# Kernel tuning notes

Measured on AMD Instinct MI355X. Metric: run time of the kernel, lower is better.

Reference implementation:

```python
import jax, jax.numpy as jnp
import numpy as np
from jax import lax

N = 100000   # total nodes in batched graph
E = 3200000  # total edges
B = 32       # graphs in batch
L = 1000     # text sequence length (required by mx3 kernel=108)
D = 128      # emb_dim
H = 3        # heads of gcn1
OD = 128     # output_dim


def setup_inputs() -> dict:
    key = jax.random.key(0)
    ks = jax.random.split(key, 32)
    def p(i, shape, s=0.05):
        return jax.random.normal(ks[i], shape, jnp.float32) * s
    return {
        "node_feat": p(0, (N, D), 1.0),
        "src": jax.random.randint(ks[1], (E,), 0, N),
        "dst": jax.random.randint(ks[2], (E,), 0, N),
        "graph_ids": jnp.sort(jax.random.randint(ks[3], (N,), 0, B)),
        "pad_dmap": p(4, (B, 1, L, D), 1.0),
        # GATConv 1: in=D, out=D, heads=3
        "W1": p(5, (D, H * D)), "al1": p(6, (H, D)), "ar1": p(7, (H, D)), "b1": p(8, (H * D,)),
        # GATConv 2: in=3D, out=3D, heads=1
        "W2": p(9, (H * D, H * D)), "al2": p(10, (1, H * D)), "ar2": p(11, (1, H * D)), "b2": p(12, (H * D,)),
        "fc_g1_w": p(13, (H * D, OD)), "fc_g1_b": p(14, (OD,)),
        # Conv1d weights in torch OIH layout
        "conv1_w": p(15, (128, D, 3)), "conv1_b": p(16, (128,)),
        "conv2_w": p(17, (128, 128, 3)), "conv2_b": p(18, (128,)),
        "conv3_w": p(19, (128, 128, 3)), "conv3_b": p(20, (128,)),
        "tf_w": p(21, (128, OD)), "tf_b": p(22, (OD,)),
        "w1": jnp.array([0.5], jnp.float32),
        "fc1_w": p(23, (OD, 512)), "fc1_b": p(24, (512,)),
        "fc2_w": p(25, (512, 256)), "fc2_b": p(26, (256,)),
        "out_w": p(27, (256, 2)), "out_b": p(28, (2,)),
    }


def _gat(feat, src, dst, W, al, ar, b, heads, od):
    """DGL GATConv (feat_drop=attn_drop=0, negative_slope=0.2, bias)."""
    n = feat.shape[0]
    h = (feat @ W).reshape(n, heads, od)                 # [N,H,od]
    el = jnp.einsum('nhd,hd->nh', h, al)                 # [N,H]
    er = jnp.einsum('nhd,hd->nh', h, ar)
    e = jax.nn.leaky_relu(el[src] + er[dst], 0.2)        # [E,H] per-edge score
    m = jax.ops.segment_max(e, dst, num_segments=n)
    m = jnp.where(jnp.isfinite(m), m, 0.0)               # isolated nodes -> 0
    a = jnp.exp(e - m[dst])
    s = jax.ops.segment_sum(a, dst, num_segments=n)
    alpha = a / s[dst]                                   # edge softmax over in-neighborhood
    rst = jax.ops.segment_sum(alpha[:, :, None] * h[src], dst, num_segments=n)
    return rst + b.reshape(1, heads, od)


def _conv1d(x, w, b):
    y = lax.conv_general_dilated(x, w, (1,), 'VALID', dimension_numbers=('NCH', 'OIH', 'NCH'))
    return y + b[None, :, None]


def _maxpool1d(x, k, s):
    return lax.reduce_window(x, -jnp.inf, lax.max, (1, 1, k), (1, 1, s), 'VALID')


def reference(node_feat, src, dst, graph_ids, pad_dmap,
              W1, al1, ar1, b1, W2, al2, ar2, b2,
              fc_g1_w, fc_g1_b, conv1_w, conv1_b, conv2_w, conv2_b,
              conv3_w, conv3_b, tf_w, tf_b, w1,
              fc1_w, fc1_b, fc2_w, fc2_b, out_w, out_b):
    relu = jax.nn.relu
    # graph branch
    g = relu(_gat(node_feat, src, dst, W1, al1, ar1, b1, H, D)).reshape(-1, H * D)
    g = relu(_gat(g, src, dst, W2, al2, ar2, b2, 1, H * D)).reshape(-1, H * D)
    gpool = jax.ops.segment_max(g, graph_ids, num_segments=B)   # graph max pooling [B,384]
    g1 = relu(gpool @ fc_g1_w + fc_g1_b)
    # text CNN branch
    x = pad_dmap[:, 0].transpose(0, 2, 1)                       # [B, D, L]
    f = _maxpool1d(_conv1d(x, conv1_w, conv1_b), 3, 3)
    f = _maxpool1d(_conv1d(f, conv2_w, conv2_b), 3, 3)
    f = _maxpool1d(_conv1d(f, conv3_w, conv3_b), 108, 1)[:, :, 0]  # [B,128]
    seq1 = relu(f @ tf_w + tf_b)
    # weighted fusion + MLP head (dropout is identity in eval)
    wv = jax.nn.sigmoid(w1)
    gc = (1.0 - wv) * g1 + wv * seq1
    gc = relu(gc @ fc1_w + fc1_b)
    gc = relu(gc @ fc2_w + fc2_b)
    o = relu(gc @ out_w + out_b)
    return jax.nn.softmax(o, axis=1)
```

## Files before the change

kernel.cpp:

```cpp
#include <hip/hip_runtime.h>
#include <math.h>

constexpr int NN = 100000;
constexpr int EE = 3200000;
constexpr int BB = 32;
constexpr int LSEQ = 1000;
constexpr int DD = 128;
constexpr int NH = 3;
constexpr int HD = 384;
constexpr int NB1 = (NN + 255) / 256;
constexpr int NMT = (NN + 127) / 128;

typedef __attribute__((ext_vector_type(8))) short bf16v8;
typedef __attribute__((ext_vector_type(4))) float f32x4;

static __device__ __forceinline__ float lrelu(float x) { return x > 0.f ? x : 0.2f * x; }
static __device__ __forceinline__ float bf2f(unsigned short u) {
  return __uint_as_float(((unsigned)u) << 16);
}
static __device__ __forceinline__ unsigned short f2bf(float f) {
  unsigned x = __float_as_uint(f);
  return (unsigned short)((x + 0x7fffu + ((x >> 16) & 1u)) >> 16);
}

constexpr int PB_NF   = (NN * DD / 4) / 256;
constexpr int PB_PAD  = (BB * LSEQ * 128 / 4) / 256;
constexpr int PB_DEG  = NB1;
constexpr int PB_GP   = (BB * HD + 255) / 256;
constexpr int PB_TW1  = (128 * 384 + 255) / 256;
constexpr int PB_TW2  = (384 * 384 + 255) / 256;
constexpr int PB_TC   = (128 * 384 + 255) / 256;
constexpr int PREP_BLOCKS = PB_NF + PB_PAD + PB_DEG + PB_GP + PB_TW1 + PB_TW2 + 3 * PB_TC;

__global__ void prep_misc(const float* __restrict__ nf, unsigned short* __restrict__ nfbf,
                          const float* __restrict__ pad, unsigned short* __restrict__ padbf,
                          int* __restrict__ deg, unsigned* __restrict__ gpool,
                          const float* __restrict__ W1, unsigned short* __restrict__ Wt1,
                          const float* __restrict__ W2, unsigned short* __restrict__ Wt2,
                          const float* __restrict__ c1w, unsigned short* __restrict__ Wc1,
                          const float* __restrict__ c2w, unsigned short* __restrict__ Wc2,
                          const float* __restrict__ c3w, unsigned short* __restrict__ Wc3) {
  int bx = blockIdx.x, tid = threadIdx.x;
  if (bx < PB_NF) {
    int i = bx * 256 + tid;
    float4 v = ((const float4*)nf)[i];
    ushort4 o;
    o.x = f2bf(v.x); o.y = f2bf(v.y); o.z = f2bf(v.z); o.w = f2bf(v.w);
    ((ushort4*)nfbf)[i] = o;
    return;
  }
  bx -= PB_NF;
  if (bx < PB_PAD) {
    int i = bx * 256 + tid;
    float4 v = ((const float4*)pad)[i];
    ushort4 o;
    o.x = f2bf(v.x); o.y = f2bf(v.y); o.z = f2bf(v.z); o.w = f2bf(v.w);
    ((ushort4*)padbf)[i] = o;
    return;
  }
  bx -= PB_PAD;
  if (bx < PB_DEG) {
    int i = bx * 256 + tid;
    if (i < NN) deg[i] = 0;
    return;
  }
  bx -= PB_DEG;
  if (bx < PB_GP) {
    int i = bx * 256 + tid;
    if (i < BB * HD) gpool[i] = 0u;
    return;
  }
  bx -= PB_GP;
  if (bx < PB_TW1) {
    int id = bx * 256 + tid;
    if (id < 384 * 128) { int n = id / 128, k = id % 128; Wt1[id] = f2bf(W1[(size_t)k * 384 + n]); }
    return;
  }
  bx -= PB_TW1;
  if (bx < PB_TW2) {
    int id = bx * 256 + tid;
    if (id < 384 * 384) { int n = id / 384, k = id % 384; Wt2[id] = f2bf(W2[(size_t)k * 384 + n]); }
    return;
  }
  bx -= PB_TW2;
  const float* cw = (bx < PB_TC) ? c1w : (bx < 2 * PB_TC) ? c2w : c3w;
  unsigned short* co = (bx < PB_TC) ? Wc1 : (bx < 2 * PB_TC) ? Wc2 : Wc3;
  int id = (bx % PB_TC) * 256 + tid;
  if (id < 128 * 384) {
    int o = id / 384, rem = id % 384;
    int t = rem / 128, i = rem % 128;
    co[id] = f2bf(cw[(size_t)o * 384 + i * 3 + t]);
  }
}

__global__ void hist_k(const int* __restrict__ dst, int* __restrict__ deg) {
  int i = blockIdx.x * 256 + threadIdx.x;
  if (i >= EE / 4) return;
  int4 d = ((const int4*)dst)[i];
  atomicAdd(&deg[d.x], 1);
  atomicAdd(&deg[d.y], 1);
  atomicAdd(&deg[d.z], 1);
  atomicAdd(&deg[d.w], 1);
}

__global__ void scan1_k(const int* __restrict__ deg, int* __restrict__ excl,
                        int* __restrict__ bsum) {
  __shared__ int tmp[256];
  int tid = threadIdx.x;
  int i = blockIdx.x * 256 + tid;
  int v = (i < NN) ? deg[i] : 0;
  tmp[tid] = v;
  __syncthreads();
  for (int off = 1; off < 256; off <<= 1) {
    int t = (tid >= off) ? tmp[tid - off] : 0;
    __syncthreads();
    tmp[tid] += t;
    __syncthreads();
  }
  if (i < NN) excl[i] = tmp[tid] - v;
  if (tid == 255) bsum[blockIdx.x] = tmp[255];
}

__global__ void scan2p(int* __restrict__ bsum) {
  __shared__ int tmp[512];
  int tid = threadIdx.x;
  int v = (tid < NB1) ? bsum[tid] : 0;
  tmp[tid] = v;
  __syncthreads();
  for (int off = 1; off < 512; off <<= 1) {
    int t = (tid >= off) ? tmp[tid - off] : 0;
    __syncthreads();
    tmp[tid] += t;
    __syncthreads();
  }
  if (tid < NB1) bsum[tid] = tmp[tid] - v;
}

__global__ void scan3_k(const int* __restrict__ excl, const int* __restrict__ bsum,
                        int* __restrict__ offs, int* __restrict__ cursor) {
  int i = blockIdx.x * 256 + threadIdx.x;
  if (i < NN) {
    int o = excl[i] + bsum[blockIdx.x];
    offs[i] = o;
    cursor[i] = o;
  }
}

__global__ void scatter_k(const int* __restrict__ src, const int* __restrict__ dst,
                          int* __restrict__ cursor, int* __restrict__ srcs) {
  int i = blockIdx.x * 256 + threadIdx.x;
  if (i >= EE / 4) return;
  int4 s = ((const int4*)src)[i];
  int4 d = ((const int4*)dst)[i];
  srcs[atomicAdd(&cursor[d.x], 1)] = s.x;
  srcs[atomicAdd(&cursor[d.y], 1)] = s.y;
  srcs[atomicAdd(&cursor[d.z], 1)] = s.z;
  srcs[atomicAdd(&cursor[d.w], 1)] = s.w;
}

template <int NKB, bool BRES>
__global__ __launch_bounds__(512) void gemm_nres(const unsigned short* __restrict__ A,
                                                 const unsigned short* __restrict__ Bt,
                                                 unsigned short* __restrict__ C,
                                                 int M, int Nc, int nmt, int mpb) {
  static_assert(!BRES || NKB <= 2, "resident B needs K<=128");
  constexpr int KTOT = NKB * 64;
  __shared__ unsigned short As[2][8192];
  __shared__ unsigned short Bs[16384];
  int tid = threadIdx.x;
  int lane = tid & 63;
  int wave = tid >> 6;
  int wm = wave >> 2, wn = wave & 3;
  int tile_n = blockIdx.x * 128;
  int rloc = lane >> 3;
  int cs = (lane & 7) ^ rloc;
  const unsigned short* Bb = Bt + (size_t)tile_n * KTOT;

  int mt0 = blockIdx.y * mpb;
  if (mt0 >= nmt) return;
  int mt1 = min(mt0 + mpb, nmt);

  auto stage_a = [&](int mt, int kb, int buf) {
    const unsigned short* Ab = A + (size_t)mt * 128 * KTOT;
    int mr = M - 1 - mt * 128;
#pragma unroll
    for (int q = 0; q < 2; ++q) {
      int t = wave * 2 + q, r = t * 8 + rloc;
      int ra = r > mr ? mr : r;
      __builtin_amdgcn_global_load_lds(
          (const __attribute__((address_space(1))) void*)(Ab + (size_t)ra * KTOT + kb * 64 + cs * 8),
          (__attribute__((address_space(3))) void*)(&As[buf][t * 512]), 16, 0, 0);
    }
  };
  auto stage_b = [&](int kb, int buf) {
#pragma unroll
    for (int q = 0; q < 2; ++q) {
      int t = wave * 2 + q, r = t * 8 + rloc;
      __builtin_amdgcn_global_load_lds(
          (const __attribute__((address_space(1))) void*)(Bb + (size_t)r * KTOT + kb * 64 + cs * 8),
          (__attribute__((address_space(3))) void*)(&Bs[buf * 8192 + t * 512]), 16, 0, 0);
    }
  };

  f32x4 acc[4][2];
#pragma unroll
  for (int i = 0; i < 4; ++i)
#pragma unroll
    for (int j = 0; j < 2; ++j) acc[i][j] = (f32x4){0.f, 0.f, 0.f, 0.f};

  if constexpr (BRES) {
#pragma unroll
    for (int kb = 0; kb < NKB; ++kb) stage_b(kb, kb);
  } else {
    stage_b(0, 0);
  }
  stage_a(mt0, 0, 0);
  __syncthreads();

  int nsteps = (mt1 - mt0) * NKB;
  for (int i = 0; i < nsteps; ++i) {
    int mt = mt0 + i / NKB;
    int kb = i % NKB;
    int cb = i & 1;
    if (i + 1 < nsteps) {
      int ni = i + 1;
      stage_a(mt0 + ni / NKB, ni % NKB, ni & 1);
      if constexpr (!BRES) stage_b(ni % NKB, ni & 1);
    }
    const unsigned short* Ablk = &As[cb][0];
    const unsigned short* Bblk = BRES ? (Bs + kb * 8192) : (Bs + cb * 8192);
#pragma unroll
    for (int ks = 0; ks < 2; ++ks) {
      int q = ks * 4 + (lane >> 4);
      bf16v8 af[4], bfr[2];
#pragma unroll
      for (int ii = 0; ii < 4; ++ii) {
        int r = wm * 64 + ii * 16 + (lane & 15);
        af[ii] = *(const bf16v8*)&Ablk[r * 64 + ((q ^ (r & 7)) * 8)];
      }
#pragma unroll
      for (int j = 0; j < 2; ++j) {
        int r = wn * 32 + j * 16 + (lane & 15);
        bfr[j] = *(const bf16v8*)&Bblk[r * 64 + ((q ^ (r & 7)) * 8)];
      }
#pragma unroll
      for (int ii = 0; ii < 4; ++ii)
#pragma unroll
        for (int j = 0; j < 2; ++j)
          acc[ii][j] = __builtin_amdgcn_mfma_f32_16x16x32_bf16(af[ii], bfr[j], acc[ii][j], 0, 0, 0);
    }
    if (kb == NKB - 1) {
#pragma unroll
      for (int ii = 0; ii < 4; ++ii) {
        int row0 = mt * 128 + wm * 64 + ii * 16 + (lane >> 4) * 4;
#pragma unroll
        for (int j = 0; j < 2; ++j) {
          int col = tile_n + wn * 32 + j * 16 + (lane & 15);
#pragma unroll
          for (int p = 0; p < 4; ++p) {
            int row = row0 + p;
            if (row < M) C[(size_t)row * Nc + col] = f2bf(acc[ii][j][p]);
          }
          acc[ii][j] = (f32x4){0.f, 0.f, 0.f, 0.f};
        }
      }
    }
    __syncthreads();
  }
}

__global__ __launch_bounds__(256) void gemm_mfma(const unsigned short* __restrict__ A,
                                                 int lda,
                                                 const unsigned short* __restrict__ Bt,
                                                 unsigned short* __restrict__ C,
                                                 int M, int K, int Nc,
                                                 const float* __restrict__ bias,
                                                 long aBatch, long cBatch) {
  __shared__ unsigned short As[128 * 64];
  __shared__ unsigned short Bs[128 * 64];
  int lane = threadIdx.x & 63;
  int wave = threadIdx.x >> 6;
  int wm = wave >> 1, wn = wave & 1;
  int tile_m = blockIdx.y * 128;
  int tile_n = blockIdx.x * 128;
  int maxRa = M - 1 - tile_m;
  f32x4 acc[4][4];
#pragma unroll
  for (int i = 0; i < 4; ++i)
#pragma unroll
    for (int j = 0; j < 4; ++j) acc[i][j] = (f32x4){0.f, 0.f, 0.f, 0.f};

  const unsigned short* Ab = A + (size_t)blockIdx.z * aBatch + (size_t)tile_m * lda;
  unsigned short* Cb = C + (size_t)blockIdx.z * cBatch;
  const unsigned short* Bb = Bt + (size_t)tile_n * K;
  int rloc = (lane >> 3);
  int cs = (lane & 7) ^ rloc;

  for (int k0 = 0; k0 < K; k0 += 64) {
#pragma unroll
    for (int q = 0; q < 4; ++q) {
      int t = wave * 4 + q;
      int r = t * 8 + rloc;
      int ra = r > maxRa ? maxRa : r;
      __builtin_amdgcn_global_load_lds(
          (const __attribute__((address_space(1))) void*)(Ab + (size_t)ra * lda + k0 + cs * 8),
          (__attribute__((address_space(3))) void*)(As + t * 512), 16, 0, 0);
      __builtin_amdgcn_global_load_lds(
          (const __attribute__((address_space(1))) void*)(Bb + (size_t)r * K + k0 + cs * 8),
          (__attribute__((address_space(3))) void*)(Bs + t * 512), 16, 0, 0);
    }
    __syncthreads();
#pragma unroll
    for (int ks = 0; ks < 2; ++ks) {
      int q = ks * 4 + (lane >> 4);
      bf16v8 af[4], bfr[4];
#pragma unroll
      for (int i = 0; i < 4; ++i) {
        int r = wm * 64 + i * 16 + (lane & 15);
        af[i] = *(const bf16v8*)&As[r * 64 + ((q ^ (r & 7)) * 8)];
      }
#pragma unroll
      for (int j = 0; j < 4; ++j) {
        int r = wn * 64 + j * 16 + (lane & 15);
        bfr[j] = *(const bf16v8*)&Bs[r * 64 + ((q ^ (r & 7)) * 8)];
      }
#pragma unroll
      for (int i = 0; i < 4; ++i)
#pragma unroll
        for (int j = 0; j < 4; ++j)
          acc[i][j] = __builtin_amdgcn_mfma_f32_16x16x32_bf16(af[i], bfr[j], acc[i][j], 0, 0, 0);
    }
    __syncthreads();
  }
#pragma unroll
  for (int i = 0; i < 4; ++i) {
    int row0 = tile_m + wm * 64 + i * 16 + (lane >> 4) * 4;
#pragma unroll
    for (int j = 0; j < 4; ++j) {
      int col = tile_n + wn * 64 + j * 16 + (lane & 15);
      float bv = bias ? bias[col] : 0.f;
#pragma unroll
      for (int p = 0; p < 4; ++p) {
        int row = row0 + p;
        if (row < M) Cb[(size_t)row * Nc + col] = f2bf(acc[i][j][p] + bv);
      }
    }
  }
}

__global__ void elr_k1(const unsigned short* __restrict__ h, const float* __restrict__ al,
                       const float* __restrict__ ar, float* __restrict__ el,
                       float* __restrict__ er) {
  int wid = (blockIdx.x * 256 + threadIdx.x) >> 6;
  int lane = threadIdx.x & 63;
  if (wid >= NN * NH) return;
  int n = wid / NH, hh = wid % NH;
  const unsigned short* row = h + (size_t)n * HD + hh * DD;
  const float* a = al + hh * DD;
  const float* r = ar + hh * DD;
  int c = lane * 2;
  unsigned v = *(const unsigned*)(row + c);
  float x0 = bf2f((unsigned short)(v & 0xffffu));
  float x1 = bf2f((unsigned short)(v >> 16));
  float pel = x0 * a[c] + x1 * a[c + 1];
  float per = x0 * r[c] + x1 * r[c + 1];
#pragma unroll
  for (int off = 32; off; off >>= 1) {
    pel += __shfl_down(pel, off);
    per += __shfl_down(per, off);
  }
  if (lane == 0) { el[n * 4 + hh] = pel; er[n * 4 + hh] = per; }
}

__global__ void elr_k2(const unsigned short* __restrict__ h, const float* __restrict__ al,
                       const float* __restrict__ ar, float* __restrict__ el,
                       float* __restrict__ er) {
  int wid = (blockIdx.x * 256 + threadIdx.x) >> 6;
  int lane = threadIdx.x & 63;
  if (wid >= NN) return;
  const unsigned short* row = h + (size_t)wid * HD;
  float pel = 0.f, per = 0.f;
#pragma unroll
  for (int k = 0; k < 3; ++k) {
    int c = lane * 2 + k * 128;
    unsigned v = *(const unsigned*)(row + c);
    float x0 = bf2f((unsigned short)(v & 0xffffu));
    float x1 = bf2f((unsigned short)(v >> 16));
    pel += x0 * al[c] + x1 * al[c + 1];
    per += x0 * ar[c] + x1 * ar[c + 1];
  }
#pragma unroll
  for (int off = 32; off; off >>= 1) {
    pel += __shfl_down(pel, off);
    per += __shfl_down(per, off);
  }
  if (lane == 0) { el[wid] = pel; er[wid] = per; }
}

template <int H>
static __device__ __forceinline__ void agg_body3(const float4 t,
                                                 const unsigned short* __restrict__ hfeat,
                                                 int lane, float acc[6]) {
  int s2 = __float_as_int(t.w);
  const unsigned short* hrow = hfeat + (size_t)s2 * HD;
  uint2 va = *(const uint2*)(hrow + lane * 4);
  unsigned vb = *(const unsigned*)(hrow + 256 + lane * 2);
  float wa = (H == 3) ? ((lane < 32) ? t.x : t.y) : t.x;
  float wc = (H == 3) ? t.z : t.x;
  acc[0] += wa * bf2f((unsigned short)(va.x & 0xffffu));
  acc[1] += wa * bf2f((unsigned short)(va.x >> 16));
  acc[2] += wa * bf2f((unsigned short)(va.y & 0xffffu));
  acc[3] += wa * bf2f((unsigned short)(va.y >> 16));
  acc[4] += wc * bf2f((unsigned short)(vb & 0xffffu));
  acc[5] += wc * bf2f((unsigned short)(vb >> 16));
}

template <int H>
static __device__ __forceinline__ void load_sc(const float* __restrict__ el,
                                               int s, const float erd[H], float sc[H]) {
  if constexpr (H == 3) {
    float4 e = ((const float4*)el)[s];
    sc[0] = lrelu(e.x + erd[0]);
    sc[1] = lrelu(e.y + erd[1]);
    sc[2] = lrelu(e.z + erd[2]);
  } else {
    sc[0] = lrelu(el[s] + erd[0]);
  }
}

template <int H>
__global__ __launch_bounds__(256) void agg_csr3(const int* __restrict__ offs,
                                                const int* __restrict__ deg,
                                                const int* __restrict__ srcs,
                                                const float* __restrict__ el,
                                                const float* __restrict__ er,
                                                const unsigned short* __restrict__ hfeat,
                                                const float* __restrict__ bias,
                                                unsigned short* __restrict__ outg) {
  __shared__ float wb[4][64][4];
  int wave = threadIdx.x >> 6, lane = threadIdx.x & 63;
  int d = blockIdx.x * 4 + wave;
  int o0 = offs[d], dg = deg[d];
  float erd[H];
  if constexpr (H == 3) {
    float4 e = ((const float4*)er)[d];
    erd[0] = e.x; erd[1] = e.y; erd[2] = e.z;
  } else {
    erd[0] = er[d];
  }
  float acc[6] = {0.f, 0.f, 0.f, 0.f, 0.f, 0.f};
  float wsum[H];
#pragma unroll
  for (int h = 0; h < H; ++h) wsum[h] = 0.f;

  if (dg <= 64) {
    bool has = lane < dg;
    int s = has ? srcs[o0 + lane] : 0;
    float sc[H], mh[H];
    load_sc<H>(el, s, erd, sc);
#pragma unroll
    for (int h = 0; h < H; ++h) {
      if (!has) sc[h] = -1e30f;
      mh[h] = sc[h];
#pragma unroll
      for (int off = 1; off < 64; off <<= 1) mh[h] = fmaxf(mh[h], __shfl_xor(mh[h], off));
    }
    float w0 = 0.f, w1 = 0.f, w2 = 0.f;
    if (has) {
      w0 = __expf(sc[0] - mh[0]);
      if constexpr (H == 3) {
        w1 = __expf(sc[1] - mh[1]);
        w2 = __expf(sc[2] - mh[2]);
      }
    }
    wsum[0] = w0;
    if constexpr (H == 3) { wsum[1] = w1; wsum[2] = w2; }
    *(float4*)&wb[wave][lane][0] = make_float4(w0, w1, w2, __int_as_float(s));
#pragma unroll 16
    for (int j = 0; j < dg; ++j) {
      float4 t = *(const float4*)&wb[wave][j][0];
      agg_body3<H>(t, hfeat, lane, acc);
    }
  } else {
    float mh[H];
#pragma unroll
    for (int h = 0; h < H; ++h) mh[h] = -1e30f;
    for (int e = lane; e < dg; e += 64) {
      int s = srcs[o0 + e];
      float sc[H];
      load_sc<H>(el, s, erd, sc);
#pragma unroll
      for (int h = 0; h < H; ++h) mh[h] = fmaxf(mh[h], sc[h]);
    }
#pragma unroll
    for (int h = 0; h < H; ++h) {
#pragma unroll
      for (int off = 1; off < 64; off <<= 1) mh[h] = fmaxf(mh[h], __shfl_xor(mh[h], off));
    }
    int nch = (dg + 63) >> 6;
    for (int ch = 0; ch < nch; ++ch) {
      int e = ch * 64 + lane;
      bool has = e < dg;
      int s = has ? srcs[o0 + e] : 0;
      float sc[H];
      load_sc<H>(el, s, erd, sc);
      float w0 = 0.f, w1 = 0.f, w2 = 0.f;
      if (has) {
        w0 = __expf(sc[0] - mh[0]);
        if constexpr (H == 3) {
          w1 = __expf(sc[1] - mh[1]);
          w2 = __expf(sc[2] - mh[2]);
        }
      }
      wsum[0] += w0;
      if constexpr (H == 3) { wsum[1] += w1; wsum[2] += w2; }
      *(float4*)&wb[wave][lane][0] = make_float4(w0, w1, w2, __int_as_float(s));
      int cnt = min(64, dg - ch * 64);
#pragma unroll 16
      for (int j = 0; j < cnt; ++j) {
        float4 t = *(const float4*)&wb[wave][j][0];
        agg_body3<H>(t, hfeat, lane, acc);
      }
    }
  }
#pragma unroll
  for (int h = 0; h < H; ++h) {
#pragma unroll
    for (int off = 1; off < 64; off <<= 1) wsum[h] += __shfl_xor(wsum[h], off);
  }
  float swA = (H == 3) ? ((lane < 32) ? wsum[0] : wsum[1]) : wsum[0];
  float swC = (H == 3) ? wsum[H - 1] : wsum[0];
  float invA = (dg > 0) ? 1.f / swA : 0.f;
  float invC = (dg > 0) ? 1.f / swC : 0.f;
  unsigned short* orow = outg + (size_t)d * HD;
  int cA = lane * 4, cB = 256 + lane * 2;
  float r0 = fmaxf(acc[0] * invA + bias[cA + 0], 0.f);
  float r1 = fmaxf(acc[1] * invA + bias[cA + 1], 0.f);
  float r2 = fmaxf(acc[2] * invA + bias[cA + 2], 0.f);
  float r3 = fmaxf(acc[3] * invA + bias[cA + 3], 0.f);
  float r4 = fmaxf(acc[4] * invC + bias[cB + 0], 0.f);
  float r5 = fmaxf(acc[5] * invC + bias[cB + 1], 0.f);
  uint2 pa;
  pa.x = (unsigned)f2bf(r0) | ((unsigned)f2bf(r1) << 16);
  pa.y = (unsigned)f2bf(r2) | ((unsigned)f2bf(r3) << 16);
  *(uint2*)(orow + cA) = pa;
  *(unsigned*)(orow + cB) = (unsigned)f2bf(r4) | ((unsigned)f2bf(r5) << 16);
}

__global__ void graph_pool(const unsigned short* __restrict__ g, const int* __restrict__ gid,
                           unsigned* __restrict__ gp) {
  int c = threadIdx.x;
  int n0 = blockIdx.x * 64;
  int nend = min(n0 + 64, NN);
  int cur = gid[n0];
  float mx = 0.f;
  for (int n = n0; n < nend; ++n) {
    int gg = gid[n];
    if (gg != cur) {
      atomicMax(&gp[cur * HD + c], __float_as_uint(mx));
      cur = gg; mx = 0.f;
    }
    mx = fmaxf(mx, bf2f(g[(size_t)n * HD + c]));
  }
  atomicMax(&gp[cur * HD + c], __float_as_uint(mx));
}

__global__ void maxpool_nhc(const unsigned short* __restrict__ in, unsigned short* __restrict__ out,
                            int Lin, int Lout, int total) {
  int idx = blockIdx.x * 256 + threadIdx.x;
  if (idx >= total) return;
  int c = idx & 127;
  int j = (idx >> 7) % Lout;
  int b = idx / (128 * Lout);
  const unsigned short* p = in + ((size_t)b * Lin + j * 3) * 128 + c;
  float m = bf2f(p[0]);
  m = fmaxf(m, bf2f(p[128]));
  m = fmaxf(m, bf2f(p[256]));
  out[idx] = f2bf(m);
}

__global__ void gpool_c3(const unsigned short* __restrict__ in, float* __restrict__ fvec) {
  int idx = blockIdx.x * 256 + threadIdx.x;
  if (idx >= BB * 128) return;
  int c = idx & 127, b = idx >> 7;
  const unsigned short* p = in + (size_t)b * 108 * 128 + c;
  float m = bf2f(p[0]);
  for (int t = 1; t < 108; ++t) m = fmaxf(m, bf2f(p[t * 128]));
  fvec[idx] = m;
}

__global__ __launch_bounds__(256) void head_all(const unsigned* __restrict__ gpool,
                                                const float* __restrict__ fvec,
                                                const float* __restrict__ fcgw,
                                                const float* __restrict__ fcgb,
                                                const float* __restrict__ tfw,
                                                const float* __restrict__ tfb,
                                                const float* __restrict__ w1s,
                                                const float* __restrict__ fc1w,
                                                const float* __restrict__ fc1b,
                                                const float* __restrict__ fc2w,
                                                const float* __restrict__ fc2b,
                                                const float* __restrict__ outw,
                                                const float* __restrict__ outb,
                                                float* __restrict__ out) {
  __shared__ float gl[HD];
  __shared__ float gcv[128];
  __shared__ float gc1[512];
  __shared__ float gc2[256];
  int b = blockIdx.x, tid = threadIdx.x;
  for (int c = tid; c < HD; c += 256) gl[c] = __uint_as_float(gpool[b * HD + c]);
  __syncthreads();
  float wv = 1.f / (1.f + __expf(-w1s[0]));
  if (tid < 128) {
    float a = fcgb[tid];
    for (int k = 0; k < HD; ++k) a += gl[k] * fcgw[(size_t)k * 128 + tid];
    float g1 = fmaxf(a, 0.f);
    float s = tfb[tid];
    const float* fv = fvec + b * 128;
    for (int k = 0; k < 128; ++k) s += fv[k] * tfw[(size_t)k * 128 + tid];
    float s1 = fmaxf(s, 0.f);
    gcv[tid] = (1.f - wv) * g1 + wv * s1;
  }
  __syncthreads();
#pragma unroll
  for (int q = 0; q < 2; ++q) {
    int j = tid + q * 256;
    float a = fc1b[j];
    for (int k = 0; k < 128; ++k) a += gcv[k] * fc1w[(size_t)k * 512 + j];
    gc1[j] = fmaxf(a, 0.f);
  }
  __syncthreads();
  {
    float a = fc2b[tid];
    for (int k = 0; k < 512; ++k) a += gc1[k] * fc2w[(size_t)k * 256 + tid];
    gc2[tid] = fmaxf(a, 0.f);
  }
  __syncthreads();
  if (tid < 64) {
    float p0 = 0.f, p1 = 0.f;
#pragma unroll
    for (int q = 0; q < 4; ++q) {
      float v = gc2[tid + q * 64];
      p0 += v * outw[(tid + q * 64) * 2 + 0];
      p1 += v * outw[(tid + q * 64) * 2 + 1];
    }
#pragma unroll
    for (int off = 32; off; off >>= 1) {
      p0 += __shfl_down(p0, off);
      p1 += __shfl_down(p1, off);
    }
    if (tid == 0) {
      float o0 = fmaxf(p0 + outb[0], 0.f), o1 = fmaxf(p1 + outb[1], 0.f);
      float mm = fmaxf(o0, o1);
      float e0 = __expf(o0 - mm), e1 = __expf(o1 - mm);
      float inv = 1.f / (e0 + e1);
      out[b * 2 + 0] = e0 * inv;
      out[b * 2 + 1] = e1 * inv;
    }
  }
}

extern "C" void kernel_launch(void* const* d_in, const int* in_sizes, int n_in,
                              void* d_out, int out_size, void* d_ws, size_t ws_size,
                              hipStream_t stream) {
  const float* node_feat = (const float*)d_in[0];
  const int*   src  = (const int*)d_in[1];
  const int*   dst  = (const int*)d_in[2];
  const int*   gids = (const int*)d_in[3];
  const float* pad  = (const float*)d_in[4];
  const float* W1   = (const float*)d_in[5];
  const float* al1  = (const float*)d_in[6];
  const float* ar1  = (const float*)d_in[7];
  const float* b1   = (const float*)d_in[8];
  const float* W2   = (const float*)d_in[9];
  const float* al2  = (const float*)d_in[10];
  const float* ar2  = (const float*)d_in[11];
  const float* b2   = (const float*)d_in[12];
  const float* fcgw = (const float*)d_in[13];
  const float* fcgb = (const float*)d_in[14];
  const float* c1w  = (const float*)d_in[15];
  const float* c1b  = (const float*)d_in[16];
  const float* c2w  = (const float*)d_in[17];
  const float* c2b  = (const float*)d_in[18];
  const float* c3w  = (const float*)d_in[19];
  const float* c3b  = (const float*)d_in[20];
  const float* tfw  = (const float*)d_in[21];
  const float* tfb  = (const float*)d_in[22];
  const float* w1s  = (const float*)d_in[23];
  const float* fc1w = (const float*)d_in[24];
  const float* fc1b = (const float*)d_in[25];
  const float* fc2w = (const float*)d_in[26];
  const float* fc2b = (const float*)d_in[27];
  const float* outw = (const float*)d_in[28];
  const float* outb = (const float*)d_in[29];
  float* out = (float*)d_out;
  char* base = (char*)d_ws;

  constexpr size_t SZ_BIG = (size_t)NN * HD * 2;
  unsigned short* hA = (unsigned short*)(base + 0);
  unsigned short* gB = (unsigned short*)(base + SZ_BIG);
  unsigned short* nfbf = gB;
  size_t o = 2 * SZ_BIG;
  unsigned short* Wt1 = (unsigned short*)(base + o); o += 384 * 128 * 2;
  unsigned short* Wt2 = (unsigned short*)(base + o); o += 384 * 384 * 2;
  unsigned short* Wc1 = (unsigned short*)(base + o); o += 128 * 384 * 2;
  unsigned short* Wc2 = (unsigned short*)(base + o); o += 128 * 384 * 2;
  unsigned short* Wc3 = (unsigned short*)(base + o); o += 128 * 384 * 2;
  int* deg    = (int*)(base + o); o += (size_t)NN * 4;
  int* offs   = (int*)(base + o); o += (size_t)NN * 4;
  int* cursor = (int*)(base + o); o += (size_t)NN * 4;
  int* excl   = (int*)(base + o); o += (size_t)NN * 4;
  int* bsum   = (int*)(base + o); o += 2048;
  int* srcs   = (int*)(base + o); o += (size_t)EE * 4;
  float* el1  = (float*)(base + o); o += (size_t)NN * 4 * 4;
  float* er1  = (float*)(base + o); o += (size_t)NN * 4 * 4;
  float* el2  = (float*)(base + o); o += (size_t)NN * 4;
  float* er2  = (float*)(base + o); o += (size_t)NN * 4;
  unsigned* gpool = (unsigned*)(base + o); o += (size_t)BB * HD * 4;
  float* fvec = (float*)(base + o); o += BB * 128 * 4;

  unsigned short* padbf = (unsigned short*)base;
  unsigned short* c1bf  = padbf + (size_t)BB * LSEQ * 128;
  unsigned short* p1bf  = c1bf + (size_t)BB * 998 * 128;
  unsigned short* c2bf  = p1bf + (size_t)BB * 332 * 128;
  unsigned short* p2bf  = c2bf + (size_t)BB * 330 * 128;
  unsigned short* c3bf  = p2bf + (size_t)BB * 110 * 128;

  prep_misc<<<PREP_BLOCKS, 256, 0, stream>>>(node_feat, nfbf, pad, padbf, deg, gpool,
                                             W1, Wt1, W2, Wt2, c1w, Wc1, c2w, Wc2, c3w, Wc3);

  gemm_mfma<<<dim3(1, 8, BB), 256, 0, stream>>>(padbf, 128, Wc1, c1bf, 998, 384, 128, c1b,
                                                (long)LSEQ * 128, (long)998 * 128);
  maxpool_nhc<<<(BB * 332 * 128 + 255) / 256, 256, 0, stream>>>(c1bf, p1bf, 998, 332, BB * 332 * 128);
  gemm_mfma<<<dim3(1, 3, BB), 256, 0, stream>>>(p1bf, 128, Wc2, c2bf, 330, 384, 128, c2b,
                                                (long)332 * 128, (long)330 * 128);
  maxpool_nhc<<<(BB * 110 * 128 + 255) / 256, 256, 0, stream>>>(c2bf, p2bf, 330, 110, BB * 110 * 128);
  gemm_mfma<<<dim3(1, 1, BB), 256, 0, stream>>>(p2bf, 128, Wc3, c3bf, 108, 384, 128, c3b,
                                                (long)110 * 128, (long)108 * 128);
  gpool_c3<<<(BB * 128 + 255) / 256, 256, 0, stream>>>(c3bf, fvec);

  hist_k<<<EE / 1024, 256, 0, stream>>>(dst, deg);
  scan1_k<<<NB1, 256, 0, stream>>>(deg, excl, bsum);
  scan2p<<<1, 512, 0, stream>>>(bsum);
  scan3_k<<<NB1, 256, 0, stream>>>(excl, bsum, offs, cursor);
  scatter_k<<<EE / 1024, 256, 0, stream>>>(src, dst, cursor, srcs);

  gemm_nres<2, true><<<dim3(3, (NMT + 9) / 10), 512, 0, stream>>>(nfbf, Wt1, hA, NN, HD, NMT, 10);
  elr_k1<<<(NN * NH * 64 + 255) / 256, 256, 0, stream>>>(hA, al1, ar1, el1, er1);
  agg_csr3<3><<<NN / 4, 256, 0, stream>>>(offs, deg, srcs, el1, er1, hA, b1, gB);

  gemm_nres<6, false><<<dim3(3, (NMT + 9) / 10), 512, 0, stream>>>(gB, Wt2, hA, NN, HD, NMT, 10);
  elr_k2<<<(NN * 64 + 255) / 256, 256, 0, stream>>>(hA, al2, ar2, el2, er2);
  agg_csr3<1><<<NN / 4, 256, 0, stream>>>(offs, deg, srcs, el2, er2, hA, b2, gB);

  graph_pool<<<(NN + 63) / 64, 384, 0, stream>>>(gB, gids, gpool);
  head_all<<<BB, 256, 0, stream>>>(gpool, fvec, fcgw, fcgb, tfw, tfb, w1s,
                                   fc1w, fc1b, fc2w, fc2b, outw, outb, out);
}
```

Before: 1.466 ms.

## Fuse attention logit projections into GEMM epilogue and drop scatter atomics via rank

The el/er attention projections are now computed in the GAT GEMM epilogue from the fp32 accumulators, using shuffle reductions and a shared-memory cross-wave sum. This removes the two separate elr kernels that re-read the bf16 hidden features. For the second layer, partial sums from the three column blocks are combined with float atomics into el2/er2, which are now zeroed in the prep kernel. Separately, the histogram kernel records each edge's atomic return value as a rank, so the scatter no longer needs atomics or a cursor array. The cost is an extra 12.8MB rank array written and read, plus an added __syncthreads and epilogue work per tile.

```diff
diff --git a/kernel.cpp b/kernel.cpp
--- a/kernel.cpp
+++ b/kernel.cpp
@@ -26,15 +26,17 @@
 constexpr int PB_NF   = (NN * DD / 4) / 256;
 constexpr int PB_PAD  = (BB * LSEQ * 128 / 4) / 256;
 constexpr int PB_DEG  = NB1;
+constexpr int PB_EL2  = (2 * NN + 255) / 256;
 constexpr int PB_GP   = (BB * HD + 255) / 256;
 constexpr int PB_TW1  = (128 * 384 + 255) / 256;
 constexpr int PB_TW2  = (384 * 384 + 255) / 256;
 constexpr int PB_TC   = (128 * 384 + 255) / 256;
-constexpr int PREP_BLOCKS = PB_NF + PB_PAD + PB_DEG + PB_GP + PB_TW1 + PB_TW2 + 3 * PB_TC;
+constexpr int PREP_BLOCKS = PB_NF + PB_PAD + PB_DEG + PB_EL2 + PB_GP + PB_TW1 + PB_TW2 + 3 * PB_TC;
 
 __global__ void prep_misc(const float* __restrict__ nf, unsigned short* __restrict__ nfbf,
                           const float* __restrict__ pad, unsigned short* __restrict__ padbf,
-                          int* __restrict__ deg, unsigned* __restrict__ gpool,
+                          int* __restrict__ deg, float* __restrict__ el2z,
+                          unsigned* __restrict__ gpool,
                           const float* __restrict__ W1, unsigned short* __restrict__ Wt1,
                           const float* __restrict__ W2, unsigned short* __restrict__ Wt2,
                           const float* __restrict__ c1w, unsigned short* __restrict__ Wc1,
@@ -65,6 +67,12 @@
     return;
   }
   bx -= PB_DEG;
+  if (bx < PB_EL2) {
+    int i = bx * 256 + tid;
+    if (i < 2 * NN) el2z[i] = 0.f;
+    return;
+  }
+  bx -= PB_EL2;
   if (bx < PB_GP) {
     int i = bx * 256 + tid;
     if (i < BB * HD) gpool[i] = 0u;
@@ -93,14 +101,17 @@
   }
 }
 
-__global__ void hist_k(const int* __restrict__ dst, int* __restrict__ deg) {
+__global__ void hist_k(const int* __restrict__ dst, int* __restrict__ deg,
+                       int* __restrict__ rank) {
   int i = blockIdx.x * 256 + threadIdx.x;
   if (i >= EE / 4) return;
   int4 d = ((const int4*)dst)[i];
-  atomicAdd(&deg[d.x], 1);
-  atomicAdd(&deg[d.y], 1);
-  atomicAdd(&deg[d.z], 1);
-  atomicAdd(&deg[d.w], 1);
+  int4 r;
+  r.x = atomicAdd(&deg[d.x], 1);
+  r.y = atomicAdd(&deg[d.y], 1);
+  r.z = atomicAdd(&deg[d.z], 1);
+  r.w = atomicAdd(&deg[d.w], 1);
+  ((int4*)rank)[i] = r;
 }
 
 __global__ void scan1_k(const int* __restrict__ deg, int* __restrict__ excl,
@@ -137,36 +148,40 @@
 }
 
 __global__ void scan3_k(const int* __restrict__ excl, const int* __restrict__ bsum,
-                        int* __restrict__ offs, int* __restrict__ cursor) {
+                        int* __restrict__ offs) {
   int i = blockIdx.x * 256 + threadIdx.x;
-  if (i < NN) {
-    int o = excl[i] + bsum[blockIdx.x];
-    offs[i] = o;
-    cursor[i] = o;
-  }
+  if (i < NN) offs[i] = excl[i] + bsum[blockIdx.x];
 }
 
 __global__ void scatter_k(const int* __restrict__ src, const int* __restrict__ dst,
-                          int* __restrict__ cursor, int* __restrict__ srcs) {
+                          const int* __restrict__ rank, const int* __restrict__ offs,
+                          int* __restrict__ srcs) {
   int i = blockIdx.x * 256 + threadIdx.x;
   if (i >= EE / 4) return;
   int4 s = ((const int4*)src)[i];
   int4 d = ((const int4*)dst)[i];
-  srcs[atomicAdd(&cursor[d.x], 1)] = s.x;
-  srcs[atomicAdd(&cursor[d.y], 1)] = s.y;
-  srcs[atomicAdd(&cursor[d.z], 1)] = s.z;
-  srcs[atomicAdd(&cursor[d.w], 1)] = s.w;
+  int4 r = ((const int4*)rank)[i];
+  srcs[offs[d.x] + r.x] = s.x;
+  srcs[offs[d.y] + r.y] = s.y;
+  srcs[offs[d.z] + r.z] = s.z;
+  srcs[offs[d.w] + r.w] = s.w;
 }
 
 template <int NKB, bool BRES>
 __global__ __launch_bounds__(512) void gemm_nres(const unsigned short* __restrict__ A,
                                                  const unsigned short* __restrict__ Bt,
                                                  unsigned short* __restrict__ C,
+                                                 const float* __restrict__ al,
+                                                 const float* __restrict__ ar,
+                                                 float* __restrict__ el,
+                                                 float* __restrict__ er,
                                                  int M, int Nc, int nmt, int mpb) {
   static_assert(!BRES || NKB <= 2, "resident B needs K<=128");
   constexpr int KTOT = NKB * 64;
   __shared__ unsigned short As[2][8192];
   __shared__ unsigned short Bs[16384];
+  __shared__ float elbuf[128][4];
+  __shared__ float erbuf[128][4];
   int tid = threadIdx.x;
   int lane = tid & 63;
   int wave = tid >> 6;
@@ -175,6 +190,10 @@
   int rloc = lane >> 3;
   int cs = (lane & 7) ^ rloc;
   const unsigned short* Bb = Bt + (size_t)tile_n * KTOT;
+
+  int c0 = tile_n + wn * 32 + (lane & 15);
+  float alv0 = al[c0], alv1 = al[c0 + 16];
+  float arv0 = ar[c0], arv1 = ar[c0 + 16];
 
   int mt0 = blockIdx.y * mpb;
   if (mt0 >= nmt) return;
@@ -261,9 +280,45 @@
             int row = row0 + p;
             if (row < M) C[(size_t)row * Nc + col] = f2bf(acc[ii][j][p]);
           }
-          acc[ii][j] = (f32x4){0.f, 0.f, 0.f, 0.f};
         }
       }
+#pragma unroll
+      for (int ii = 0; ii < 4; ++ii) {
+#pragma unroll
+        for (int p = 0; p < 4; ++p) {
+          float pe = acc[ii][0][p] * alv0 + acc[ii][1][p] * alv1;
+          float pr = acc[ii][0][p] * arv0 + acc[ii][1][p] * arv1;
+#pragma unroll
+          for (int off = 1; off < 16; off <<= 1) {
+            pe += __shfl_xor(pe, off);
+            pr += __shfl_xor(pr, off);
+          }
+          if ((lane & 15) == 0) {
+            int rl = wm * 64 + ii * 16 + (lane >> 4) * 4 + p;
+            elbuf[rl][wn] = pe;
+            erbuf[rl][wn] = pr;
+          }
+        }
+      }
+      __syncthreads();
+      if (tid < 128) {
+        int row = mt * 128 + tid;
+        if (row < M) {
+          float ev = elbuf[tid][0] + elbuf[tid][1] + elbuf[tid][2] + elbuf[tid][3];
+          float rv = erbuf[tid][0] + erbuf[tid][1] + erbuf[tid][2] + erbuf[tid][3];
+          if constexpr (BRES) {
+            el[row * 4 + blockIdx.x] = ev;
+            er[row * 4 + blockIdx.x] = rv;
+          } else {
+            atomicAdd(&el[row], ev);
+            atomicAdd(&er[row], rv);
+          }
+        }
+      }
+#pragma unroll
+      for (int ii = 0; ii < 4; ++ii)
+#pragma unroll
+        for (int j = 0; j < 2; ++j) acc[ii][j] = (f32x4){0.f, 0.f, 0.f, 0.f};
     }
     __syncthreads();
   }
@@ -346,55 +401,6 @@
       }
     }
   }
-}
-
-__global__ void elr_k1(const unsigned short* __restrict__ h, const float* __restrict__ al,
-                       const float* __restrict__ ar, float* __restrict__ el,
-                       float* __restrict__ er) {
-  int wid = (blockIdx.x * 256 + threadIdx.x) >> 6;
-  int lane = threadIdx.x & 63;
-  if (wid >= NN * NH) return;
-  int n = wid / NH, hh = wid % NH;
-  const unsigned short* row = h + (size_t)n * HD + hh * DD;
-  const float* a = al + hh * DD;
-  const float* r = ar + hh * DD;
-  int c = lane * 2;
-  unsigned v = *(const unsigned*)(row + c);
-  float x0 = bf2f((unsigned short)(v & 0xffffu));
-  float x1 = bf2f((unsigned short)(v >> 16));
-  float pel = x0 * a[c] + x1 * a[c + 1];
-  float per = x0 * r[c] + x1 * r[c + 1];
-#pragma unroll
-  for (int off = 32; off; off >>= 1) {
-    pel += __shfl_down(pel, off);
-    per += __shfl_down(per, off);
-  }
-  if (lane == 0) { el[n * 4 + hh] = pel; er[n * 4 + hh] = per; }
-}
-
-__global__ void elr_k2(const unsigned short* __restrict__ h, const float* __restrict__ al,
-                       const float* __restrict__ ar, float* __restrict__ el,
-                       float* __restrict__ er) {
-  int wid = (blockIdx.x * 256 + threadIdx.x) >> 6;
-  int lane = threadIdx.x & 63;
-  if (wid >= NN) return;
-  const unsigned short* row = h + (size_t)wid * HD;
-  float pel = 0.f, per = 0.f;
-#pragma unroll
-  for (int k = 0; k < 3; ++k) {
-    int c = lane * 2 + k * 128;
-    unsigned v = *(const unsigned*)(row + c);
-    float x0 = bf2f((unsigned short)(v & 0xffffu));
-    float x1 = bf2f((unsigned short)(v >> 16));
-    pel += x0 * al[c] + x1 * al[c + 1];
-    per += x0 * ar[c] + x1 * ar[c + 1];
-  }
-#pragma unroll
-  for (int off = 32; off; off >>= 1) {
-    pel += __shfl_down(pel, off);
-    per += __shfl_down(per, off);
-  }
-  if (lane == 0) { el[wid] = pel; er[wid] = per; }
 }
 
 template <int H>
@@ -708,10 +714,10 @@
   unsigned short* Wc3 = (unsigned short*)(base + o); o += 128 * 384 * 2;
   int* deg    = (int*)(base + o); o += (size_t)NN * 4;
   int* offs   = (int*)(base + o); o += (size_t)NN * 4;
-  int* cursor = (int*)(base + o); o += (size_t)NN * 4;
   int* excl   = (int*)(base + o); o += (size_t)NN * 4;
   int* bsum   = (int*)(base + o); o += 2048;
   int* srcs   = (int*)(base + o); o += (size_t)EE * 4;
+  int* rank   = (int*)(base + o); o += (size_t)EE * 4;
   float* el1  = (float*)(base + o); o += (size_t)NN * 4 * 4;
   float* er1  = (float*)(base + o); o += (size_t)NN * 4 * 4;
   float* el2  = (float*)(base + o); o += (size_t)NN * 4;
@@ -726,7 +732,7 @@
   unsigned short* p2bf  = c2bf + (size_t)BB * 330 * 128;
   unsigned short* c3bf  = p2bf + (size_t)BB * 110 * 128;
 
-  prep_misc<<<PREP_BLOCKS, 256, 0, stream>>>(node_feat, nfbf, pad, padbf, deg, gpool,
+  prep_misc<<<PREP_BLOCKS, 256, 0, stream>>>(node_feat, nfbf, pad, padbf, deg, el2, gpool,
                                              W1, Wt1, W2, Wt2, c1w, Wc1, c2w, Wc2, c3w, Wc3);
 
   gemm_mfma<<<dim3(1, 8, BB), 256, 0, stream>>>(padbf, 128, Wc1, c1bf, 998, 384, 128, c1b,
@@ -739,18 +745,18 @@
                                                 (long)110 * 128, (long)108 * 128);
   gpool_c3<<<(BB * 128 + 255) / 256, 256, 0, stream>>>(c3bf, fvec);
 
-  hist_k<<<EE / 1024, 256, 0, stream>>>(dst, deg);
+  hist_k<<<EE / 1024, 256, 0, stream>>>(dst, deg, rank);
   scan1_k<<<NB1, 256, 0, stream>>>(deg, excl, bsum);
   scan2p<<<1, 512, 0, stream>>>(bsum);
-  scan3_k<<<NB1, 256, 0, stream>>>(excl, bsum, offs, cursor);
-  scatter_k<<<EE / 1024, 256, 0, stream>>>(src, dst, cursor, srcs);
-
-  gemm_nres<2, true><<<dim3(3, (NMT + 9) / 10), 512, 0, stream>>>(nfbf, Wt1, hA, NN, HD, NMT, 10);
-  elr_k1<<<(NN * NH * 64 + 255) / 256, 256, 0, stream>>>(hA, al1, ar1, el1, er1);
+  scan3_k<<<NB1, 256, 0, stream>>>(excl, bsum, offs);
+  scatter_k<<<EE / 1024, 256, 0, stream>>>(src, dst, rank, offs, srcs);
+
+  gemm_nres<2, true><<<dim3(3, (NMT + 9) / 10), 512, 0, stream>>>(
+      nfbf, Wt1, hA, al1, ar1, el1, er1, NN, HD, NMT, 10);
   agg_csr3<3><<<NN / 4, 256, 0, stream>>>(offs, deg, srcs, el1, er1, hA, b1, gB);
 
-  gemm_nres<6, false><<<dim3(3, (NMT + 9) / 10), 512, 0, stream>>>(gB, Wt2, hA, NN, HD, NMT, 10);
-  elr_k2<<<(NN * 64 + 255) / 256, 256, 0, stream>>>(hA, al2, ar2, el2, er2);
+  gemm_nres<6, false><<<dim3(3, (NMT + 9) / 10), 512, 0, stream>>>(
+      gB, Wt2, hA, al2, ar2, el2, er2, NN, HD, NMT, 10);
   agg_csr3<1><<<NN / 4, 256, 0, stream>>>(offs, deg, srcs, el2, er2, hA, b2, gB);
 
   graph_pool<<<(NN + 63) / 64, 384, 0, stream>>>(gB, gids, gpool);
```

Result: faster. 1.264 ms (-13.8%).
